# Performance work log

Hardware: AMD Instinct MI355X
Metric: run time of the kernel (lower is better)

## Reference

```python
import jax, jax.numpy as jnp
import numpy as np

L, C, H = 4, 512, 8
HD = C // H

def silu(x):
    return x * jax.nn.sigmoid(x)

def layernorm(x, g, b, eps=1e-5):
    m = x.mean(-1, keepdims=True)
    v = ((x - m) ** 2).mean(-1, keepdims=True)
    return (x - m) * jax.lax.rsqrt(v + eps) * g + b

def adaln(x, t, w, b):
    # x: (N,B,C), t: (B,C), w: (2C,C), b: (2C,)
    mod = silu(t) @ w.T + b
    scale, shift = jnp.split(mod, 2, axis=-1)
    return x * (1.0 + scale[None]) + shift[None]

def embed_rotary(x, pos):
    # x: (B,N,C), pos: (B,N,C,2) with [...,0]=cos, [...,1]=sin
    cos, sin = pos[..., 0], pos[..., 1]
    x2 = jnp.stack([-x[..., 1::2], x[..., 0::2]], axis=-1).reshape(x.shape)
    return x * cos + x2 * sin

def setup_inputs() -> dict:
    key = jax.random.key(0)
    ks = jax.random.split(key, 24)
    Nq, Nkv, B = 1024, 2048, 4
    query = jax.random.normal(ks[0], (Nq, B, C), jnp.float32)
    value = jax.random.normal(ks[1], (Nkv, B, C), jnp.float32)
    diff_ts = jax.random.normal(ks[2], (B, C), jnp.float32)
    # valid rotary codes: cos/sin of random angles
    aq = jax.random.uniform(ks[3], (B, Nq, C), jnp.float32, 0.0, 2 * np.pi)
    ak = jax.random.uniform(ks[4], (B, Nkv, C), jnp.float32, 0.0, 2 * np.pi)
    query_pos = jnp.stack([jnp.cos(aq), jnp.sin(aq)], axis=-1)
    value_pos = jnp.stack([jnp.cos(ak), jnp.sin(ak)], axis=-1)
    s = 0.02
    inp = dict(query=query, value=value, diff_ts=diff_ts,
               query_pos=query_pos, value_pos=value_pos,
               aw_attn=jax.random.normal(ks[5], (L, 2 * C, C)) * s,
               ab_attn=jax.random.normal(ks[6], (L, 2 * C)) * s,
               in_w=jax.random.normal(ks[7], (L, 3 * C, C)) * s,
               in_b=jnp.zeros((L, 3 * C)),
               out_w=jax.random.normal(ks[8], (L, C, C)) * s,
               out_b=jnp.zeros((L, C)),
               ln1_g=jnp.ones((L, C)), ln1_b=jnp.zeros((L, C)),
               aw_ffn=jax.random.normal(ks[9], (L, 2 * C, C)) * s,
               ab_ffn=jax.random.normal(ks[10], (L, 2 * C)) * s,
               w1=jax.random.normal(ks[11], (L, C, C)) * s,
               b1=jnp.zeros((L, C)),
               w2=jax.random.normal(ks[12], (L, C, C)) * s,
               b2=jnp.zeros((L, C)),
               ln2_g=jnp.ones((L, C)), ln2_b=jnp.zeros((L, C)))
    return inp

def _forward(query, value, diff_ts, query_pos, value_pos,
             aw_attn, ab_attn, in_w, in_b, out_w, out_b, ln1_g, ln1_b,
             aw_ffn, ab_ffn, w1, b1, w2, b2, ln2_g, ln2_b):
    Nq, B, _ = query.shape
    Nkv = value.shape[0]
    scaling = HD ** -0.5
    outputs = []
    q = query
    for i in range(L):
        # --- cross-attention layer ---
        aq = adaln(q, diff_ts, aw_attn[i], ab_attn[i])
        wq, wk, wv = jnp.split(in_w[i], 3, axis=0)
        bq, bk, bv = jnp.split(in_b[i], 3, axis=0)
        qp = (aq @ wq.T + bq) * scaling          # (Nq,B,C)
        kp = value @ wk.T + bk                    # (Nkv,B,C)
        vp = value @ wv.T + bv
        qb = embed_rotary(qp.transpose(1, 0, 2), query_pos)  # (B,Nq,C)
        kb = embed_rotary(kp.transpose(1, 0, 2), value_pos)  # (B,Nkv,C)
        vb = vp.transpose(1, 0, 2)
        qh = qb.reshape(B, Nq, H, HD).transpose(0, 2, 1, 3)   # (B,H,Nq,HD)
        kh = kb.reshape(B, Nkv, H, HD).transpose(0, 2, 1, 3)
        vh = vb.reshape(B, Nkv, H, HD).transpose(0, 2, 1, 3)
        scores = jnp.einsum('bhqd,bhkd->bhqk', qh, kh)
        attn = jax.nn.softmax(scores, axis=-1)
        o = jnp.einsum('bhqk,bhkd->bhqd', attn, vh)
        o = o.transpose(0, 2, 1, 3).reshape(B, Nq, C).transpose(1, 0, 2)  # (Nq,B,C)
        o = o @ out_w[i].T + out_b[i]
        q = layernorm(q + o, ln1_g[i], ln1_b[i])
        # --- feedforward layer (residual uses AdaLN-modulated x) ---
        xa = adaln(q, diff_ts, aw_ffn[i], ab_ffn[i])
        h = jax.nn.relu(xa @ w1[i].T + b1[i])
        h = h @ w2[i].T + b2[i]
        q = layernorm(xa + h, ln2_g[i], ln2_b[i])
        outputs.append(q)
    return jnp.stack(outputs)  # (L, Nq, B, C)

def reference(query, value, diff_ts, query_pos, value_pos,
              aw_attn, ab_attn, in_w, in_b, out_w, out_b, ln1_g, ln1_b,
              aw_ffn, ab_ffn, w1, b1, w2, b2, ln2_g, ln2_b):
    return _forward(query, value, diff_ts, query_pos, value_pos,
                    aw_attn, ab_attn, in_w, in_b, out_w, out_b, ln1_g, ln1_b,
                    aw_ffn, ab_ffn, w1, b1, w2, b2, ln2_g, ln2_b)
```

## Files before the change

### kernel.cpp

```cpp
#include <hip/hip_runtime.h>
#include <hip/hip_bf16.h>

typedef __hip_bfloat16 bf16;
typedef __attribute__((ext_vector_type(8))) short short8;
typedef __attribute__((ext_vector_type(4))) short s16x4;
typedef __attribute__((ext_vector_type(4))) float f32x4;

#define CDIM 512
#define BDIM 4
#define HDIM 8
#define HDQ  64
#define NQ   1024
#define NKV  2048
#define LAYERS 4
#define SPLIT 2

#if defined(__has_builtin)
#if __has_builtin(__builtin_amdgcn_global_load_lds)
#define USE_GLL 1
#endif
#endif

static __device__ __forceinline__ short f2s(float f) {
    bf16 h = __float2bfloat16(f);
    return *reinterpret_cast<short*>(&h);
}


__global__ __launch_bounds__(256) void convall_k(
    const float* __restrict__ s0, const float* __restrict__ s1,
    const float* __restrict__ s2, const float* __restrict__ s3,
    const float* __restrict__ s4,
    bf16* __restrict__ d0, bf16* __restrict__ d1, bf16* __restrict__ d2,
    bf16* __restrict__ d3, bf16* __restrict__ d4) {
    int gid = blockIdx.x * 256 + threadIdx.x;
    const float* src; bf16* dst; int off;
    if (gid < 1048576)      { src = s0; dst = d0; off = gid; }
    else if (gid < 1835008) { src = s1; dst = d1; off = gid - 1048576; }
    else if (gid < 2097152) { src = s2; dst = d2; off = gid - 1835008; }
    else if (gid < 2359296) { src = s3; dst = d3; off = gid - 2097152; }
    else                    { src = s4; dst = d4; off = gid - 2359296; }
    f32x4 v = *(const f32x4*)(src + (size_t)off * 4);
    s16x4 o;
    o[0] = f2s(v[0]); o[1] = f2s(v[1]); o[2] = f2s(v[2]); o[3] = f2s(v[3]);
    *(s16x4*)(dst + (size_t)off * 4) = o;
}

__global__ __launch_bounds__(256) void modall_k(const float* __restrict__ diff_ts,
    const float* __restrict__ aw_attn, const float* __restrict__ ab_attn,
    const float* __restrict__ aw_ffn,  const float* __restrict__ ab_ffn,
    float* __restrict__ mod) {
    int wv = blockIdx.x * 4 + (threadIdx.x >> 6);
    int lane = threadIdx.x & 63;
    int col  = wv & 1023;
    int b    = (wv >> 10) & 3;
    int kind = (wv >> 12) & 1;
    int l    = wv >> 13;
    const float* w = (kind ? aw_ffn : aw_attn) + ((size_t)l * 1024 + col) * CDIM + lane * 8;
    const float* tb = diff_ts + b * CDIM + lane * 8;
    f32x4 w0 = *(const f32x4*)w;
    f32x4 w1 = *(const f32x4*)(w + 4);
    f32x4 t0 = *(const f32x4*)tb;
    f32x4 t1 = *(const f32x4*)(tb + 4);
    #pragma unroll
    for (int j = 0; j < 4; ++j) {
        t0[j] = t0[j] / (1.f + __expf(-t0[j]));
        t1[j] = t1[j] / (1.f + __expf(-t1[j]));
    }
    f32x4 pp = w0 * t0 + w1 * t1;
    float acc = (pp[0] + pp[1]) + (pp[2] + pp[3]);
    #pragma unroll
    for (int off = 32; off; off >>= 1) acc += __shfl_xor(acc, off);
    if (lane == 0)
        mod[wv] = acc + (kind ? ab_ffn : ab_attn)[l * 1024 + col];
}

__global__ __launch_bounds__(256) void adaln_k(const float* __restrict__ x,
                                               const float* __restrict__ mod,
                                               bf16* __restrict__ outb) {
    int i = blockIdx.x * 256 + threadIdx.x;
    int c = i & 511;
    int b = (i >> 9) & 3;
    outb[i] = __float2bfloat16(x[i] * (1.f + mod[b * 1024 + c]) + mod[b * 1024 + 512 + c]);
}

__global__ __launch_bounds__(256) void ln_ad_k(const float* __restrict__ x,
                                               const float* __restrict__ res,
                                               const float* __restrict__ g,
                                               const float* __restrict__ bb,
                                               const float* __restrict__ mod,
                                               float* __restrict__ ln_f,
                                               float* __restrict__ ln_f2,
                                               float* __restrict__ ad_f,
                                               bf16* __restrict__ ad_b) {
    int row = blockIdx.x;
    int t = threadIdx.x;
    size_t base = (size_t)row * CDIM;
    float v0 = x[base + t] + res[base + t];
    float v1 = x[base + t + 256] + res[base + t + 256];
    float s1 = v0 + v1;
    float s2 = v0 * v0 + v1 * v1;
    #pragma unroll
    for (int off = 32; off; off >>= 1) {
        s1 += __shfl_xor(s1, off);
        s2 += __shfl_xor(s2, off);
    }
    __shared__ float a1[4], a2[4];
    int w = t >> 6;
    if ((t & 63) == 0) { a1[w] = s1; a2[w] = s2; }
    __syncthreads();
    s1 = a1[0] + a1[1] + a1[2] + a1[3];
    s2 = a2[0] + a2[1] + a2[2] + a2[3];
    float mean = s1 * (1.f / 512.f);
    float var = s2 * (1.f / 512.f) - mean * mean;
    float rs = rsqrtf(var + 1e-5f);
    float y0 = (v0 - mean) * rs * g[t] + bb[t];
    float y1 = (v1 - mean) * rs * g[t + 256] + bb[t + 256];
    if (ln_f)  { ln_f[base + t] = y0;  ln_f[base + t + 256] = y1; }
    if (ln_f2) { ln_f2[base + t] = y0; ln_f2[base + t + 256] = y1; }
    if (mod) {
        int b = row & 3;
        float o0 = y0 * (1.f + mod[b * 1024 + t]) + mod[b * 1024 + 512 + t];
        float o1 = y1 * (1.f + mod[b * 1024 + t + 256]) + mod[b * 1024 + 512 + t + 256];
        if (ad_f) { ad_f[base + t] = o0; ad_f[base + t + 256] = o1; }
        ad_b[base + t] = __float2bfloat16(o0);
        ad_b[base + t + 256] = __float2bfloat16(o1);
    }
}

template <int EPI, int WM, int NT, bool SWZ>
__global__ __launch_bounds__(256) void mgemm_k(
    const bf16* __restrict__ A, const bf16* __restrict__ Wt,
    const float* __restrict__ bias, void* __restrict__ out0v,
    int M, int N, int K,
    const float* __restrict__ pos, float scl, int Nseq) {
    __shared__ bf16 As[2][2][64 * 32];
    __shared__ bf16 Bs[2][2][64 * 32];
    int t = threadIdx.x;
    int w = t >> 6;
    int lane = t & 63;
    int l16 = lane & 15;
    int quad = lane >> 4;
    int wy = w >> 1, wx = w & 1;

    int bxi, byi;
    if (SWZ) {
        int nx = gridDim.x, ny = gridDim.y;
        int flat = blockIdx.y * nx + blockIdx.x;
        int nwg = nx * ny;
        int s = (flat & 7) * (nwg >> 3) + (flat >> 3);
        bxi = s % nx; byi = s / nx;
    } else {
        bxi = blockIdx.x; byi = blockIdx.y;
    }
    int bm = byi * 64;
    int bn = bxi * 64;

    int lr2 = lane >> 2;
    int lc4 = (lane & 3) ^ ((lane >> 3) & 3);

    f32x4 acc[WM][NT] = {};

    auto stage = [&](int buf, int k0) {
#if USE_GLL
        const bf16* sa = A + (size_t)(bm + w * 16 + lr2) * K + k0 + lc4 * 8;
        const bf16* sb = Wt + (size_t)(bn + w * 16 + lr2) * K + k0 + lc4 * 8;
        #pragma unroll
        for (int j = 0; j < 2; ++j) {
            __builtin_amdgcn_global_load_lds(
                (const unsigned int __attribute__((address_space(1)))*)(sa + j * 32),
                (unsigned int __attribute__((address_space(3)))*)(&As[buf][j][w * 512]),
                16, 0, 0);
            __builtin_amdgcn_global_load_lds(
                (const unsigned int __attribute__((address_space(1)))*)(sb + j * 32),
                (unsigned int __attribute__((address_space(3)))*)(&Bs[buf][j][w * 512]),
                16, 0, 0);
        }
#else
        for (int e = t; e < 512; e += 256) {
            int sub = e >> 8, c = e & 255;
            int row = c >> 2, c4 = c & 3;
            int srcc = c4 ^ ((row >> 1) & 3);
            *(uint4*)&As[buf][sub][row * 32 + c4 * 8] =
                *(const uint4*)(A + (size_t)(bm + row) * K + k0 + sub * 32 + srcc * 8);
            *(uint4*)&Bs[buf][sub][row * 32 + c4 * 8] =
                *(const uint4*)(Wt + (size_t)(bn + row) * K + k0 + sub * 32 + srcc * 8);
        }
#endif
    };

    stage(0, 0);
    int cur = 0;
    int rchunk = (quad ^ ((l16 >> 1) & 3)) * 8;

    for (int k0 = 0; k0 < K; k0 += 64) {
        bool more = (k0 + 64 < K);
        if (more) stage(cur ^ 1, k0 + 64);
#if USE_GLL
        if (more) asm volatile("s_waitcnt vmcnt(4)" ::: "memory");
        else      asm volatile("s_waitcnt vmcnt(0)" ::: "memory");
        __builtin_amdgcn_s_barrier();
#else
        __syncthreads();
#endif

        #pragma unroll
        for (int kk = 0; kk < 2; ++kk) {
            short8 af[WM], bfr[NT];
            #pragma unroll
            for (int mt = 0; mt < WM; ++mt)
                af[mt] = *(const short8*)
                    &As[cur][kk][((wy * WM + mt) * 16 + l16) * 32 + rchunk];
            #pragma unroll
            for (int nt = 0; nt < NT; ++nt)
                bfr[nt] = *(const short8*)
                    &Bs[cur][kk][((wx * NT + nt) * 16 + l16) * 32 + rchunk];
            #pragma unroll
            for (int mt = 0; mt < WM; ++mt)
                #pragma unroll
                for (int nt = 0; nt < NT; ++nt)
                    acc[mt][nt] = __builtin_amdgcn_mfma_f32_16x16x32_bf16(
                        af[mt], bfr[nt], acc[mt][nt], 0, 0, 0);
        }

#if USE_GLL
        __builtin_amdgcn_s_barrier();
#else
        __syncthreads();
#endif
        cur ^= 1;
    }

    #pragma unroll
    for (int nt = 0; nt < NT; ++nt) {
        int n = bn + (wx * NT + nt) * 16 + l16;
        float bnv = bias[n];
        #pragma unroll
        for (int mt = 0; mt < WM; ++mt) {
            #pragma unroll
            for (int r = 0; r < 4; ++r) {
                int m = bm + (wy * WM + mt) * 16 + quad * 4 + r;
                float v = acc[mt][nt][r] + bnv;
                if (EPI == 0) {
                    ((float*)out0v)[(size_t)m * N + n] = v;
                } else {
                    ((bf16*)out0v)[(size_t)m * N + n] = __float2bfloat16(fmaxf(v, 0.f));
                }
            }
        }
    }
}

__global__ __launch_bounds__(512) void qkv8_k(
    const bf16* __restrict__ a_bf, const bf16* __restrict__ val,
    const bf16* __restrict__ winb_i, const float* __restrict__ in_b_i,
    bf16* __restrict__ qh, bf16* __restrict__ kh, bf16* __restrict__ vt,
    const float* __restrict__ qpos, const float* __restrict__ vpos,
    float scaling) {
    __shared__ bf16 As[2][2][128 * 32];
    __shared__ bf16 B0[2][2][64 * 32];
    __shared__ bf16 B1[2][2][64 * 32];
    int t = threadIdx.x;
    int w = t >> 6;
    int lane = t & 63;
    int l16 = lane & 15;
    int quad = lane >> 4;
    int wy = w >> 1, wx = w & 1;
    const int K = CDIM;

    bool isq = (blockIdx.x >= 512);
    int bm, bn;
    const bf16 *Aptr, *W0, *W1;
    if (isq) {
        int flat = blockIdx.x - 512;
        int s = (flat & 7) * 32 + (flat >> 3);
        bn = (s & 7) * 64; bm = (s >> 3) * 128;
        Aptr = a_bf; W0 = winb_i; W1 = nullptr;
    } else {
        int flat = blockIdx.x;
        int s = (flat & 7) * 64 + (flat >> 3);
        bn = (s & 7) * 64; bm = (s >> 3) * 128;
        Aptr = val; W0 = winb_i + (size_t)512 * CDIM; W1 = winb_i + (size_t)1024 * CDIM;
    }

    int lr2 = lane >> 2;
    int lc4 = (lane & 3) ^ ((lane >> 3) & 3);

    auto stage = [&](int buf, int k0) {
#if USE_GLL
        const bf16* sa = Aptr + (size_t)(bm + w * 16 + lr2) * K + k0 + lc4 * 8;
        #pragma unroll
        for (int j = 0; j < 2; ++j) {
            __builtin_amdgcn_global_load_lds(
                (const unsigned int __attribute__((address_space(1)))*)(sa + j * 32),
                (unsigned int __attribute__((address_space(3)))*)(&As[buf][j][w * 512]),
                16, 0, 0);
        }
        if (w < 4) {
            const bf16* sk = W0 + (size_t)(bn + w * 16 + lr2) * K + k0 + lc4 * 8;
            #pragma unroll
            for (int j = 0; j < 2; ++j) {
                __builtin_amdgcn_global_load_lds(
                    (const unsigned int __attribute__((address_space(1)))*)(sk + j * 32),
                    (unsigned int __attribute__((address_space(3)))*)(&B0[buf][j][w * 512]),
                    16, 0, 0);
            }
        } else if (!isq) {
            const bf16* sv = W1 + (size_t)(bn + (w - 4) * 16 + lr2) * K + k0 + lc4 * 8;
            #pragma unroll
            for (int j = 0; j < 2; ++j) {
                __builtin_amdgcn_global_load_lds(
                    (const unsigned int __attribute__((address_space(1)))*)(sv + j * 32),
                    (unsigned int __attribute__((address_space(3)))*)(&B1[buf][j][(w - 4) * 512]),
                    16, 0, 0);
            }
        }
#else
        for (int u = t; u < 1024; u += 512) {
            int sub = u >> 9, c = u & 511;
            int row = c >> 2, c4 = c & 3;
            int srcc = c4 ^ ((row >> 1) & 3);
            *(uint4*)&As[buf][sub][row * 32 + c4 * 8] =
                *(const uint4*)(Aptr + (size_t)(bm + row) * K + k0 + sub * 32 + srcc * 8);
        }
        {
            int u = t;
            int sub = u >> 8, c = u & 255;
            int row = c >> 2, c4 = c & 3;
            int srcc = c4 ^ ((row >> 1) & 3);
            *(uint4*)&B0[buf][sub][row * 32 + c4 * 8] =
                *(const uint4*)(W0 + (size_t)(bn + row) * K + k0 + sub * 32 + srcc * 8);
            if (!isq)
                *(uint4*)&B1[buf][sub][row * 32 + c4 * 8] =
                    *(const uint4*)(W1 + (size_t)(bn + row) * K + k0 + sub * 32 + srcc * 8);
        }
#endif
    };

    int rchunk = (quad ^ ((l16 >> 1) & 3)) * 8;
    stage(0, 0);
    int cur = 0;

    if (isq) {
        f32x4 acc[2][2] = {};
        for (int k0 = 0; k0 < K; k0 += 64) {
            bool more = (k0 + 64 < K);
            if (more) stage(cur ^ 1, k0 + 64);
#if USE_GLL
            if (more) {
                if (w < 4) asm volatile("s_waitcnt vmcnt(4)" ::: "memory");
                else       asm volatile("s_waitcnt vmcnt(2)" ::: "memory");
            } else {
                asm volatile("s_waitcnt vmcnt(0)" ::: "memory");
            }
            __builtin_amdgcn_s_barrier();
#else
            __syncthreads();
#endif
            #pragma unroll
            for (int kk = 0; kk < 2; ++kk) {
                short8 af[2], bfr[2];
                #pragma unroll
                for (int mt = 0; mt < 2; ++mt)
                    af[mt] = *(const short8*)
                        &As[cur][kk][(wy * 32 + mt * 16 + l16) * 32 + rchunk];
                #pragma unroll
                for (int nt = 0; nt < 2; ++nt)
                    bfr[nt] = *(const short8*)
                        &B0[cur][kk][((wx * 2 + nt) * 16 + l16) * 32 + rchunk];
                #pragma unroll
                for (int mt = 0; mt < 2; ++mt)
                    #pragma unroll
                    for (int nt = 0; nt < 2; ++nt)
                        acc[mt][nt] = __builtin_amdgcn_mfma_f32_16x16x32_bf16(
                            af[mt], bfr[nt], acc[mt][nt], 0, 0, 0);
            }
#if USE_GLL
            __builtin_amdgcn_s_barrier();
#else
            __syncthreads();
#endif
            cur ^= 1;
        }

        #pragma unroll
        for (int nt = 0; nt < 2; ++nt) {
            int n = bn + (wx * 2 + nt) * 16 + l16;
            float bnv = in_b_i[n];
            #pragma unroll
            for (int mt = 0; mt < 2; ++mt) {
                #pragma unroll
                for (int r = 0; r < 4; ++r) {
                    int m = bm + wy * 32 + mt * 16 + quad * 4 + r;
                    float v = (acc[mt][nt][r] + bnv) * scaling;
                    int nseq = m >> 2, b = m & 3;
                    float part = __shfl_xor(v, 1);
                    const float* pp = qpos + (((size_t)b * NQ + nseq) * CDIM + n) * 2;
                    float cs = pp[0], sn = pp[1];
                    float o = (l16 & 1) ? (v * cs + part * sn) : (v * cs - part * sn);
                    qh[((size_t)(b * HDIM + (n >> 6)) * NQ + nseq) * HDQ + (n & 63)] =
                        __float2bfloat16(o);
                }
            }
        }
    } else {
        f32x4 acck[2][2] = {};
        f32x4 accv[2][2] = {};
        for (int k0 = 0; k0 < K; k0 += 64) {
            bool more = (k0 + 64 < K);
            if (more) stage(cur ^ 1, k0 + 64);
#if USE_GLL
            if (more) asm volatile("s_waitcnt vmcnt(4)" ::: "memory");
            else      asm volatile("s_waitcnt vmcnt(0)" ::: "memory");
            __builtin_amdgcn_s_barrier();
#else
            __syncthreads();
#endif
            #pragma unroll
            for (int kk = 0; kk < 2; ++kk) {
                short8 af[2], bkf[2], bvf[2];
                #pragma unroll
                for (int mt = 0; mt < 2; ++mt)
                    af[mt] = *(const short8*)
                        &As[cur][kk][(wy * 32 + mt * 16 + l16) * 32 + rchunk];
                #pragma unroll
                for (int nt = 0; nt < 2; ++nt) {
                    bkf[nt] = *(const short8*)
                        &B0[cur][kk][((wx * 2 + nt) * 16 + l16) * 32 + rchunk];
                    bvf[nt] = *(const short8*)
                        &B1[cur][kk][((wx * 2 + nt) * 16 + l16) * 32 + rchunk];
                }
                #pragma unroll
                for (int mt = 0; mt < 2; ++mt)
                    #pragma unroll
                    for (int nt = 0; nt < 2; ++nt) {
                        acck[mt][nt] = __builtin_amdgcn_mfma_f32_16x16x32_bf16(
                            af[mt], bkf[nt], acck[mt][nt], 0, 0, 0);
                        accv[mt][nt] = __builtin_amdgcn_mfma_f32_16x16x32_bf16(
                            af[mt], bvf[nt], accv[mt][nt], 0, 0, 0);
                    }
            }
#if USE_GLL
            __builtin_amdgcn_s_barrier();
#else
            __syncthreads();
#endif
            cur ^= 1;
        }

        #pragma unroll
        for (int nt = 0; nt < 2; ++nt) {
            int n = bn + (wx * 2 + nt) * 16 + l16;
            float bk_n = in_b_i[512 + n];
            float bv_n = in_b_i[1024 + n];
            int d = n & 63, hh = n >> 6;
            #pragma unroll
            for (int mt = 0; mt < 2; ++mt) {
                #pragma unroll
                for (int r = 0; r < 4; ++r) {
                    int m = bm + wy * 32 + mt * 16 + quad * 4 + r;
                    int nseq = m >> 2, b = m & 3;
                    float v = acck[mt][nt][r] + bk_n;
                    float part = __shfl_xor(v, 1);
                    const float* pp = vpos + (((size_t)b * NKV + nseq) * CDIM + n) * 2;
                    float cs = pp[0], sn = pp[1];
                    float o = (l16 & 1) ? (v * cs + part * sn) : (v * cs - part * sn);
                    kh[((size_t)(b * HDIM + hh) * NKV + nseq) * HDQ + d] =
                        __float2bfloat16(o);
                    float vv = accv[mt][nt][r] + bv_n;
                    vt[((size_t)(b * HDIM + hh) * HDQ + d) * NKV + nseq] =
                        __float2bfloat16(vv);
                }
            }
        }
    }
}

__global__ __launch_bounds__(512) void attn8_k(const bf16* __restrict__ qh,
                                               const bf16* __restrict__ kh,
                                               const bf16* __restrict__ vT,
                                               float* __restrict__ pl,
                                               float* __restrict__ pacc) {
    __shared__ short Kb[2][64 * 64];
    __shared__ short Vb[2][64 * 64];
    __shared__ short Ps[8][16 * 64];
    int t = threadIdx.x;
    int wave = t >> 6, lane = t & 63;
    int l16 = lane & 15, quad = lane >> 4;

    int b0 = blockIdx.x;
    int newid = (b0 & 7) * 64 + (b0 >> 3);
    int qtile = newid & 7;
    int grp = newid >> 3;
    int split = grp & 1;
    int bh = grp >> 1;
    int q0 = qtile * 128 + wave * 16;
    int kbase = split * (NKV / SPLIT);

    const bf16* qbase = qh + ((size_t)bh * NQ + q0) * HDQ;
    short8 aq0 = *(const short8*)(qbase + (size_t)l16 * HDQ + quad * 8);
    short8 aq1 = *(const short8*)(qbase + (size_t)l16 * HDQ + 32 + quad * 8);
    const bf16* kbh = kh + ((size_t)bh * NKV + kbase) * HDQ;
    const bf16* vbh = vT + (size_t)bh * HDQ * NKV + kbase;

    int r0 = wave * 8;
    int lr = lane >> 3;
    int swz_src = ((lane & 7) ^ lr) * 8;

    auto stage = [&](int buf, int kt) {
#if USE_GLL
        __builtin_amdgcn_global_load_lds(
            (const unsigned int __attribute__((address_space(1)))*)
                (kbh + (size_t)(kt + r0 + lr) * HDQ + swz_src),
            (unsigned int __attribute__((address_space(3)))*)&Kb[buf][r0 * 64],
            16, 0, 0);
        __builtin_amdgcn_global_load_lds(
            (const unsigned int __attribute__((address_space(1)))*)
                (vbh + (size_t)(r0 + lr) * NKV + kt + swz_src),
            (unsigned int __attribute__((address_space(3)))*)&Vb[buf][r0 * 64],
            16, 0, 0);
#else
        int rr = r0 + lr;
        int lc = lane & 7;
        *(short8*)&Kb[buf][rr * 64 + ((lc ^ (rr & 7)) * 8)] =
            *(const short8*)(kbh + (size_t)(kt + rr) * HDQ + lc * 8);
        *(short8*)&Vb[buf][rr * 64 + ((lc ^ (rr & 7)) * 8)] =
            *(const short8*)(vbh + (size_t)rr * NKV + kt + lc * 8);
#endif
    };

    f32x4 accO[4] = {};
    float lsum[4] = {0.f, 0.f, 0.f, 0.f};

    stage(0, 0);
    int cur = 0;
    int swz_m = l16 & 7;

    for (int kt = 0; kt < NKV / SPLIT; kt += 64) {
        bool more = (kt + 64 < NKV / SPLIT);
        if (more) stage(cur ^ 1, kt + 64);
#if USE_GLL
        if (more) asm volatile("s_waitcnt vmcnt(2)" ::: "memory");
        else      asm volatile("s_waitcnt vmcnt(0)" ::: "memory");
        __builtin_amdgcn_s_barrier();
#else
        __syncthreads();
#endif

        f32x4 sc[4] = {};
        #pragma unroll
        for (int nt = 0; nt < 4; ++nt) {
            const short* kr = &Kb[cur][(nt * 16 + l16) * 64];
            short8 bk0 = *(const short8*)&kr[(quad ^ swz_m) * 8];
            short8 bk1 = *(const short8*)&kr[((quad + 4) ^ swz_m) * 8];
            sc[nt] = __builtin_amdgcn_mfma_f32_16x16x32_bf16(aq0, bk0, sc[nt], 0, 0, 0);
            sc[nt] = __builtin_amdgcn_mfma_f32_16x16x32_bf16(aq1, bk1, sc[nt], 0, 0, 0);
        }

        #pragma unroll
        for (int r = 0; r < 4; ++r) {
            float p0 = exp2f(sc[0][r]);
            float p1 = exp2f(sc[1][r]);
            float p2 = exp2f(sc[2][r]);
            float p3 = exp2f(sc[3][r]);
            lsum[r] += (p0 + p1) + (p2 + p3);
            int pr = quad * 4 + r;
            short* prow = &Ps[wave][pr * 64];
            int pm = pr & 7;
            int ch = l16 >> 3, kl = l16 & 7;
            prow[((ch ^ pm) << 3) + kl]       = f2s(p0);
            prow[(((ch + 2) ^ pm) << 3) + kl] = f2s(p1);
            prow[(((ch + 4) ^ pm) << 3) + kl] = f2s(p2);
            prow[(((ch + 6) ^ pm) << 3) + kl] = f2s(p3);
        }

        const short* prd = &Ps[wave][l16 * 64];
        short8 pa0 = *(const short8*)&prd[(quad ^ swz_m) * 8];
        short8 pa1 = *(const short8*)&prd[((quad + 4) ^ swz_m) * 8];
        #pragma unroll
        for (int nt = 0; nt < 4; ++nt) {
            const short* vr = &Vb[cur][(nt * 16 + l16) * 64];
            short8 bv0 = *(const short8*)&vr[(quad ^ swz_m) * 8];
            short8 bv1 = *(const short8*)&vr[((quad + 4) ^ swz_m) * 8];
            accO[nt] = __builtin_amdgcn_mfma_f32_16x16x32_bf16(pa0, bv0, accO[nt], 0, 0, 0);
            accO[nt] = __builtin_amdgcn_mfma_f32_16x16x32_bf16(pa1, bv1, accO[nt], 0, 0, 0);
        }

#if USE_GLL
        __builtin_amdgcn_s_barrier();
#else
        __syncthreads();
#endif
        cur ^= 1;
    }

    #pragma unroll
    for (int r = 0; r < 4; ++r) {
        #pragma unroll
        for (int off = 1; off < 16; off <<= 1) lsum[r] += __shfl_xor(lsum[r], off);
    }

    size_t rowbase = ((size_t)split * 32 + bh) * NQ + q0;
    #pragma unroll
    for (int r = 0; r < 4; ++r) {
        size_t row = rowbase + quad * 4 + r;
        if (l16 == 0) pl[row] = lsum[r];
        #pragma unroll
        for (int nt = 0; nt < 4; ++nt)
            pacc[row * 64 + nt * 16 + l16] = accO[nt][r];
    }
}

__global__ __launch_bounds__(256) void attn_comb_k(const float* __restrict__ pl,
                                                   const float* __restrict__ pacc,
                                                   bf16* __restrict__ o) {
    int idx = blockIdx.x * 256 + threadIdx.x;
    int d4 = (idx & 15) << 2;
    int row = idx >> 4;
    int q = row & (NQ - 1);
    int bh = row >> 10;
    const int S = 32 * NQ;
    float rl = 1.0f / (pl[row] + pl[S + row]);
    f32x4 a = *(const f32x4*)&pacc[(size_t)row * 64 + d4];
    f32x4 b = *(const f32x4*)&pacc[(size_t)(S + row) * 64 + d4];
    int bsel = bh >> 3, h = bh & 7;
    s16x4 o4;
    #pragma unroll
    for (int j = 0; j < 4; ++j) o4[j] = f2s((a[j] + b[j]) * rl);
    *(s16x4*)&o[((size_t)(q * BDIM + bsel)) * CDIM + h * HDQ + d4] = o4;
}


extern "C" void kernel_launch(void* const* d_in, const int* in_sizes, int n_in,
                              void* d_out, int out_size, void* d_ws, size_t ws_size,
                              hipStream_t stream) {
    const float* query     = (const float*)d_in[0];
    const float* value     = (const float*)d_in[1];
    const float* diff_ts   = (const float*)d_in[2];
    const float* query_pos = (const float*)d_in[3];
    const float* value_pos = (const float*)d_in[4];
    const float* aw_attn   = (const float*)d_in[5];
    const float* ab_attn   = (const float*)d_in[6];
    const float* in_w      = (const float*)d_in[7];
    const float* in_b      = (const float*)d_in[8];
    const float* out_w     = (const float*)d_in[9];
    const float* out_b     = (const float*)d_in[10];
    const float* ln1_g     = (const float*)d_in[11];
    const float* ln1_b     = (const float*)d_in[12];
    const float* aw_ffn    = (const float*)d_in[13];
    const float* ab_ffn    = (const float*)d_in[14];
    const float* w1        = (const float*)d_in[15];
    const float* b1        = (const float*)d_in[16];
    const float* w2        = (const float*)d_in[17];
    const float* b2        = (const float*)d_in[18];
    const float* ln2_g     = (const float*)d_in[19];
    const float* ln2_b     = (const float*)d_in[20];
    float* out_f = (float*)d_out;

    float* ws      = (float*)d_ws;
    float* mod_ws  = ws + 2048;
    float* q_cur   = ws + 34816;
    float* buf_a   = q_cur + 2097152;
    float* buf_p   = buf_a + 2097152;
    bf16* a_bf     = (bf16*)(buf_p + 2097152);
    bf16* h_bf     = a_bf + 2097152;
    bf16* qh       = h_bf + 2097152;
    bf16* kh       = qh + 2097152;
    bf16* vt       = kh + 4194304;
    bf16* val_bf   = vt + 4194304;
    bf16* winb     = val_bf + 4194304;
    bf16* woutb    = winb + 3145728;
    bf16* w1b      = woutb + 1048576;
    bf16* w2b      = w1b + 1048576;
    float* pacc    = buf_a;
    float* pl      = (float*)a_bf;

    const int MQ = NQ * BDIM;
    const float scaling = 0.125f * 1.44269504f;

    modall_k<<<8192, 256, 0, stream>>>(diff_ts, aw_attn, ab_attn, aw_ffn, ab_ffn, mod_ws);
    convall_k<<<10240, 256, 0, stream>>>(value, in_w, out_w, w1, w2,
                                         val_bf, winb, woutb, w1b, w2b);
    adaln_k<<<(MQ * CDIM) / 256, 256, 0, stream>>>(query, mod_ws, a_bf);

    for (int i = 0; i < LAYERS; ++i) {
        const float* mod_ffn  = mod_ws + i * 8192 + 4096;
        const float* mod_attn_next = (i + 1 < LAYERS) ? (mod_ws + (i + 1) * 8192) : nullptr;
        const bf16* winb_i = winb + (size_t)i * 1536 * CDIM;
        const float* in_b_i = in_b + (size_t)i * 1536;
        const float* qsrc = (i == 0) ? query : q_cur;

        qkv8_k<<<768, 512, 0, stream>>>(a_bf, val_bf, winb_i, in_b_i,
                                        qh, kh, vt, query_pos, value_pos, scaling);
        attn8_k<<<512, 512, 0, stream>>>(qh, kh, vt, pl, pacc);
        attn_comb_k<<<2048, 256, 0, stream>>>(pl, pacc, h_bf);
        mgemm_k<0, 2, 2, true><<<dim3(8, MQ / 64), 256, 0, stream>>>(
            h_bf, woutb + (size_t)i * CDIM * CDIM, out_b + i * CDIM, buf_p,
            MQ, 512, CDIM, nullptr, 0.f, 0);
        ln_ad_k<<<MQ, 256, 0, stream>>>(qsrc, buf_p,
                                        ln1_g + i * CDIM, ln1_b + i * CDIM,
                                        mod_ffn, nullptr, nullptr, buf_a, a_bf);
        mgemm_k<1, 2, 2, true><<<dim3(8, MQ / 64), 256, 0, stream>>>(
            a_bf, w1b + (size_t)i * CDIM * CDIM, b1 + i * CDIM, h_bf,
            MQ, 512, CDIM, nullptr, 0.f, 0);
        mgemm_k<0, 2, 2, true><<<dim3(8, MQ / 64), 256, 0, stream>>>(
            h_bf, w2b + (size_t)i * CDIM * CDIM, b2 + i * CDIM, buf_p,
            MQ, 512, CDIM, nullptr, 0.f, 0);
        ln_ad_k<<<MQ, 256, 0, stream>>>(buf_a, buf_p,
                                        ln2_g + i * CDIM, ln2_b + i * CDIM,
                                        mod_attn_next, q_cur,
                                        out_f + (size_t)i * MQ * CDIM, nullptr, a_bf);
    }
}
```

Before: 633.2 us.

## Split-K the out-proj and FFN2 GEMMs, summing partials in layernorm

The output-projection and second FFN GEMMs now run as split-K with two K halves on gridDim.z. Each half writes an fp32 partial to its own buffer, and only the first half adds the bias. The following layernorm kernel takes an extra residual pointer and sums both partials, so no atomics or separate reduction kernel are needed. This doubles the block count of small GEMMs (512 blocks) to fill more CUs, at the cost of an extra 8 MB fp32 write and read per GEMM.

```diff
diff --git a/kernel.cpp b/kernel.cpp
--- a/kernel.cpp
+++ b/kernel.cpp
@@ -86,6 +86,7 @@
 
 __global__ __launch_bounds__(256) void ln_ad_k(const float* __restrict__ x,
                                                const float* __restrict__ res,
+                                               const float* __restrict__ res2,
                                                const float* __restrict__ g,
                                                const float* __restrict__ bb,
                                                const float* __restrict__ mod,
@@ -98,6 +99,10 @@
     size_t base = (size_t)row * CDIM;
     float v0 = x[base + t] + res[base + t];
     float v1 = x[base + t + 256] + res[base + t + 256];
+    if (res2) {
+        v0 += res2[base + t];
+        v1 += res2[base + t + 256];
+    }
     float s1 = v0 + v1;
     float s2 = v0 * v0 + v1 * v1;
     #pragma unroll
@@ -128,11 +133,11 @@
     }
 }
 
-template <int EPI, int WM, int NT, bool SWZ>
+template <int EPI, int WM, int NT, bool SWZ, int KS>
 __global__ __launch_bounds__(256) void mgemm_k(
     const bf16* __restrict__ A, const bf16* __restrict__ Wt,
     const float* __restrict__ bias, void* __restrict__ out0v,
-    int M, int N, int K,
+    void* __restrict__ out1v, int M, int N, int K,
     const float* __restrict__ pos, float scl, int Nseq) {
     __shared__ bf16 As[2][2][64 * 32];
     __shared__ bf16 Bs[2][2][64 * 32];
@@ -156,6 +161,9 @@
     int bm = byi * 64;
     int bn = bxi * 64;
 
+    int kbeg = 0, kend = K;
+    if (KS == 2) { int half = K >> 1; kbeg = blockIdx.z * half; kend = kbeg + half; }
+
     int lr2 = lane >> 2;
     int lc4 = (lane & 3) ^ ((lane >> 3) & 3);
 
@@ -189,12 +197,12 @@
 #endif
     };
 
-    stage(0, 0);
+    stage(0, kbeg);
     int cur = 0;
     int rchunk = (quad ^ ((l16 >> 1) & 3)) * 8;
 
-    for (int k0 = 0; k0 < K; k0 += 64) {
-        bool more = (k0 + 64 < K);
+    for (int k0 = kbeg; k0 < kend; k0 += 64) {
+        bool more = (k0 + 64 < kend);
         if (more) stage(cur ^ 1, k0 + 64);
 #if USE_GLL
         if (more) asm volatile("s_waitcnt vmcnt(4)" ::: "memory");
@@ -231,10 +239,11 @@
         cur ^= 1;
     }
 
+    float* fout = (KS == 2 && blockIdx.z) ? (float*)out1v : (float*)out0v;
     #pragma unroll
     for (int nt = 0; nt < NT; ++nt) {
         int n = bn + (wx * NT + nt) * 16 + l16;
-        float bnv = bias[n];
+        float bnv = (KS == 2 && blockIdx.z) ? 0.f : bias[n];
         #pragma unroll
         for (int mt = 0; mt < WM; ++mt) {
             #pragma unroll
@@ -242,7 +251,7 @@
                 int m = bm + (wy * WM + mt) * 16 + quad * 4 + r;
                 float v = acc[mt][nt][r] + bnv;
                 if (EPI == 0) {
-                    ((float*)out0v)[(size_t)m * N + n] = v;
+                    fout[(size_t)m * N + n] = v;
                 } else {
                     ((bf16*)out0v)[(size_t)m * N + n] = __float2bfloat16(fmaxf(v, 0.f));
                 }
@@ -672,6 +681,7 @@
     bf16* woutb    = winb + 3145728;
     bf16* w1b      = woutb + 1048576;
     bf16* w2b      = w1b + 1048576;
+    float* buf_p2  = (float*)(w2b + 1048576);
     float* pacc    = buf_a;
     float* pl      = (float*)a_bf;
 
@@ -694,19 +704,19 @@
                                         qh, kh, vt, query_pos, value_pos, scaling);
         attn8_k<<<512, 512, 0, stream>>>(qh, kh, vt, pl, pacc);
         attn_comb_k<<<2048, 256, 0, stream>>>(pl, pacc, h_bf);
-        mgemm_k<0, 2, 2, true><<<dim3(8, MQ / 64), 256, 0, stream>>>(
-            h_bf, woutb + (size_t)i * CDIM * CDIM, out_b + i * CDIM, buf_p,
+        mgemm_k<0, 2, 2, true, 2><<<dim3(8, MQ / 64, 2), 256, 0, stream>>>(
+            h_bf, woutb + (size_t)i * CDIM * CDIM, out_b + i * CDIM, buf_p, buf_p2,
             MQ, 512, CDIM, nullptr, 0.f, 0);
-        ln_ad_k<<<MQ, 256, 0, stream>>>(qsrc, buf_p,
+        ln_ad_k<<<MQ, 256, 0, stream>>>(qsrc, buf_p, buf_p2,
                                         ln1_g + i * CDIM, ln1_b + i * CDIM,
                                         mod_ffn, nullptr, nullptr, buf_a, a_bf);
-        mgemm_k<1, 2, 2, true><<<dim3(8, MQ / 64), 256, 0, stream>>>(
-            a_bf, w1b + (size_t)i * CDIM * CDIM, b1 + i * CDIM, h_bf,
+        mgemm_k<1, 2, 2, true, 1><<<dim3(8, MQ / 64), 256, 0, stream>>>(
+            a_bf, w1b + (size_t)i * CDIM * CDIM, b1 + i * CDIM, h_bf, nullptr,
             MQ, 512, CDIM, nullptr, 0.f, 0);
-        mgemm_k<0, 2, 2, true><<<dim3(8, MQ / 64), 256, 0, stream>>>(
-            h_bf, w2b + (size_t)i * CDIM * CDIM, b2 + i * CDIM, buf_p,
+        mgemm_k<0, 2, 2, true, 2><<<dim3(8, MQ / 64, 2), 256, 0, stream>>>(
+            h_bf, w2b + (size_t)i * CDIM * CDIM, b2 + i * CDIM, buf_p, buf_p2,
             MQ, 512, CDIM, nullptr, 0.f, 0);
-        ln_ad_k<<<MQ, 256, 0, stream>>>(buf_a, buf_p,
+        ln_ad_k<<<MQ, 256, 0, stream>>>(buf_a, buf_p, buf_p2,
                                         ln2_g + i * CDIM, ln2_b + i * CDIM,
                                         mod_attn_next, q_cur,
                                         out_f + (size_t)i * MQ * CDIM, nullptr, a_bf);
```

Measured after the change: 656.0 us. 1.04x slower.
